# Performance work log

Hardware: AMD Instinct MI355X
Metric: run time of the kernel (lower is better)

Reference implementation:

```python
import jax, jax.numpy as jnp
import numpy as np

N, IN_DIM, E, H, L, M = 65536, 512, 128, 4, 2, 256
DH = E // H  # 32

def _gaussian_orthogonal(m, d, rng):
    # FAVOR+ gaussian orthogonal random matrix (performer_pytorch, scaling=0)
    blocks = []
    for _ in range((m + d - 1) // d):
        q, _ = np.linalg.qr(rng.normal(size=(d, d)))
        blocks.append(q.T)
    mat = np.concatenate(blocks)[:m]
    mult = np.linalg.norm(rng.normal(size=(m, d)), axis=1)
    return (mult[:, None] * mat).astype(np.float32)

def setup_inputs() -> dict:
    rng = np.random.default_rng(0)
    r = lambda *s: jnp.asarray(rng.normal(size=s, scale=0.02), jnp.float32)
    z = lambda *s: jnp.zeros(s, jnp.float32)
    o = lambda *s: jnp.ones(s, jnp.float32)
    return dict(
        x=jnp.asarray(rng.normal(size=(N, IN_DIM)), dtype=jnp.float32),
        Wpin=r(IN_DIM, E), bpin=z(E),
        lag=o(L, E), lab=z(L, E),                    # performer inner pre-LN (attn)
        Wq=r(L, E, E), Wk=r(L, E, E), Wv=r(L, E, E), # qkv (no bias in performer_pytorch)
        Wo=r(L, E, E), bo=z(L, E),                   # attn to_out
        lbg=o(L, E), lbb=z(L, E),                    # performer inner pre-LN (ff)
        Wf1=r(L, E, 4 * E), bf1=z(L, 4 * E),         # performer inner GELU FFN
        Wf2=r(L, 4 * E, E), bf2=z(L, E),
        Wpo=r(L, E, E), bpo=z(L, E),                 # PerformerSelfAttention.out_proj
        n1g=o(L, E), n1b=z(L, E),                    # block norm1
        Wn1=r(L, E, 4 * E), bn1=z(L, 4 * E),         # block ReLU FFN
        Wn2=r(L, 4 * E, E), bn2=z(L, E),
        n2g=o(L, E), n2b=z(L, E),                    # block norm2
        Wc=r(E, 1), bc=z(1),                         # classifier
        proj=jnp.stack([jnp.asarray(_gaussian_orthogonal(M, DH, rng)) for _ in range(L)]),
    )

def _ln(x, g, b, eps=1e-5):
    mu = x.mean(-1, keepdims=True)
    var = ((x - mu) ** 2).mean(-1, keepdims=True)
    return (x - mu) * jax.lax.rsqrt(var + eps) * g + b

def _softmax_kernel(data, proj, is_query, eps=1e-4):
    # data: [1,H,N,DH]; proj: [M,DH]  (performer_pytorch softmax_kernel)
    dn = data.shape[-1] ** -0.25
    ratio = proj.shape[0] ** -0.5
    dd = jnp.einsum('bhnd,md->bhnm', data * dn, proj)
    diag = (data ** 2).sum(-1, keepdims=True) * 0.5 * (dn * dn)
    stab = jnp.max(dd, -1, keepdims=True) if is_query else jnp.max(dd)
    return ratio * (jnp.exp(dd - diag - stab) + eps)

def _linear_attn(qf, kf, v):
    # non-causal FAVOR+: O(N*M*DH)
    D = jnp.einsum('bhnm,bhm->bhn', qf, kf.sum(-2))          # denominator
    ctx = jnp.einsum('bhnm,bhnd->bhmd', kf, v)               # [1,H,M,DH]
    return jnp.einsum('bhnm,bhmd->bhnd', qf, ctx) / D[..., None]

def _forward(x, Wpin, bpin, lag, lab, Wq, Wk, Wv, Wo, bo, lbg, lbb,
             Wf1, bf1, Wf2, bf2, Wpo, bpo, n1g, n1b, Wn1, bn1, Wn2, bn2,
             n2g, n2b, Wc, bc, proj):
    h = (x @ Wpin + bpin)[None]  # [1,N,E]
    split = lambda t: t.reshape(1, -1, H, DH).transpose(0, 2, 1, 3)
    for l in range(L):
        # --- inner Performer (depth=1): pre-LN attn + pre-LN GELU FFN, residuals ---
        y = _ln(h, lag[l], lab[l])
        q, k, v = split(y @ Wq[l]), split(y @ Wk[l]), split(y @ Wv[l])
        qf = _softmax_kernel(q, proj[l], True)
        kf = _softmax_kernel(k, proj[l], False)
        a = _linear_attn(qf, kf, v).transpose(0, 2, 1, 3).reshape(1, -1, E)
        h1 = h + (a @ Wo[l] + bo[l])
        y2 = _ln(h1, lbg[l], lbb[l])
        h2 = h1 + (jax.nn.gelu(y2 @ Wf1[l] + bf1[l], approximate=False) @ Wf2[l] + bf2[l])
        # --- outer block: post-LN residual attn + post-LN ReLU FFN ---
        attn_out = h2 @ Wpo[l] + bpo[l]
        h = _ln(h + attn_out, n1g[l], n1b[l])
        ffn = jax.nn.relu(h @ Wn1[l] + bn1[l]) @ Wn2[l] + bn2[l]
        h = _ln(h + ffn, n2g[l], n2b[l])
    return jax.nn.sigmoid(h[0] @ Wc + bc)[:, 0]  # [N]

def reference(x, Wpin, bpin, lag, lab, Wq, Wk, Wv, Wo, bo, lbg, lbb,
              Wf1, bf1, Wf2, bf2, Wpo, bpo, n1g, n1b, Wn1, bn1, Wn2, bn2,
              n2g, n2b, Wc, bc, proj):
    return _forward(x, Wpin, bpin, lag, lab, Wq, Wk, Wv, Wo, bo, lbg, lbb,
                    Wf1, bf1, Wf2, bf2, Wpo, bpo, n1g, n1b, Wn1, bn1, Wn2, bn2,
                    n2g, n2b, Wc, bc, proj)
```

## Files before the change

kernel.cpp:

```cpp
#include <hip/hip_runtime.h>
#include <math.h>

#define NTOK  65536
#define EDIM  128
#define HN    4
#define DHD   32
#define MF    256
#define LLAYERS 2
#define INDIM 512
#define FDIM  512
#define CR    512
#define NCHK  (NTOK/CR)

#define DN    0.4204482076268573f
#define DN2   0.17677669529663687f
#define KEPS  1e-4f

typedef unsigned short u16;
typedef unsigned int   u32;
typedef __attribute__((ext_vector_type(8))) __bf16 bf16x8;
typedef __attribute__((ext_vector_type(4))) float  f32x4;

__device__ __forceinline__ u16 f2bf(float f){
  u32 u = __float_as_uint(f);
  u32 r = (u + 0x7fffu + ((u >> 16) & 1u)) >> 16;
  return (u16)r;
}
__device__ __forceinline__ float bf2f(u16 h){ return __uint_as_float(((u32)h) << 16); }

__device__ __forceinline__ void gload_lds16(const void* g, void* l){
  __builtin_amdgcn_global_load_lds(
      (const __attribute__((address_space(1))) u32*)g,
      (__attribute__((address_space(3))) u32*)l, 16, 0, 0);
}

__device__ __forceinline__ unsigned f2ord(float f){
  unsigned u = __float_as_uint(f);
  return (u & 0x80000000u) ? ~u : (u | 0x80000000u);
}
__device__ __forceinline__ float ord2f(unsigned e){
  unsigned u = (e & 0x80000000u) ? (e & 0x7fffffffu) : ~e;
  return __uint_as_float(u);
}

struct PrepArgs {
  const float* Wpin; const float* Wq; const float* Wk; const float* Wv;
  const float* Wo;   const float* Wpo; const float* Wf1; const float* Wf2;
  const float* Wn1;  const float* Wn2; const float* proj;
};

__global__ __launch_bounds__(256) void prep_kernel(PrepArgs a, u16* __restrict__ wts,
                                                   u16* __restrict__ pjb,
                                                   unsigned* __restrict__ stabp)
{
  int idx = blockIdx.x * 256 + threadIdx.x;
  if (idx == 0) { stabp[0] = 0x007FFFFFu; stabp[1] = 0x007FFFFFu; }
  const float* sp; u16* dp; int r, K, J;
  if      (idx <  65536) { sp = a.Wpin; dp = wts;          r = idx;          K = 512; J = 128; }
  else if (idx <  98304) { sp = a.Wq;   dp = wts +  65536; r = idx -  65536; K = 128; J = 128; }
  else if (idx < 131072) { sp = a.Wk;   dp = wts +  98304; r = idx -  98304; K = 128; J = 128; }
  else if (idx < 163840) { sp = a.Wv;   dp = wts + 131072; r = idx - 131072; K = 128; J = 128; }
  else if (idx < 196608) { sp = a.Wo;   dp = wts + 163840; r = idx - 163840; K = 128; J = 128; }
  else if (idx < 229376) { sp = a.Wpo;  dp = wts + 196608; r = idx - 196608; K = 128; J = 128; }
  else if (idx < 360448) { sp = a.Wf1;  dp = wts + 229376; r = idx - 229376; K = 128; J = 512; }
  else if (idx < 491520) { sp = a.Wf2;  dp = wts + 360448; r = idx - 360448; K = 512; J = 128; }
  else if (idx < 622592) { sp = a.Wn1;  dp = wts + 491520; r = idx - 491520; K = 128; J = 512; }
  else if (idx < 753664) { sp = a.Wn2;  dp = wts + 622592; r = idx - 622592; K = 512; J = 128; }
  else { int p = idx - 753664; pjb[p] = f2bf(a.proj[p] * DN); return; }
  int kj = K * J;
  int l = r / kj, rr = r - l * kj;
  int j = rr / K, k = rr - j * K;
  dp[r] = f2bf(sp[(size_t)l * kj + (size_t)k * J + j]);
}

template<int LNM, bool A32, bool MULTI>
__global__ __launch_bounds__(256, 4) void gemm_f(
    const u16* __restrict__ A, const float* __restrict__ Af,
    const u16* __restrict__ Bt,
    const float* __restrict__ bias, const u16* __restrict__ res,
    u16* __restrict__ outRaw, int K, int J, int op,
    const float* __restrict__ g1, const float* __restrict__ b1, u16* __restrict__ outL1,
    u16* __restrict__ outAux,
    const float* __restrict__ Wcp, const float* __restrict__ bcp, float* __restrict__ outCls)
{
  __shared__ __align__(16) u16 pool[18432];
  __shared__ float lnred[2][2][32][2];
  u16* Al = pool;
  u16* Bl = pool + 6144;
  const int tid  = threadIdx.x;
  const int lane = tid & 63;
  const int w    = tid >> 6;
  const int wr   = w >> 1, wc = w & 1;
  const int n0   = blockIdx.x * 64;
  const int jb   = MULTI ? 0 : blockIdx.y * 128;
  const u16* Bu  = MULTI ? (Bt + (size_t)blockIdx.y * 32768) : Bt;

  f32x4 acc[2][4];
#pragma unroll
  for (int m = 0; m < 2; ++m)
#pragma unroll
    for (int n = 0; n < 4; ++n) acc[m][n] = (f32x4){0.f, 0.f, 0.f, 0.f};

  const int srow = lane >> 2;
  const int skg  = (lane & 3) ^ ((lane >> 3) & 3);

  auto stageB = [&](int buf, int k0) {
#pragma unroll
    for (int i = 0; i < 2; ++i) {
      const int rb = 2 * w + i;
      gload_lds16(Bu + (size_t)(jb + rb * 16 + srow) * K + k0 + skg * 8,
                  &Bl[buf * 4096 + rb * 512]);
    }
  };
  auto stageA16 = [&](int buf, int k0) {
    gload_lds16(A + (size_t)(n0 + w * 16 + srow) * K + k0 + skg * 8,
                &Al[buf * 2048 + w * 512]);
  };

  const int r16f = lane & 15;
  const int kgl  = (lane >> 4) ^ ((lane >> 1) & 3);
  const int foff = r16f * 32 + kgl * 8;

  auto compute = [&](int cur) {
    bf16x8 af[2], bfg[4];
#pragma unroll
    for (int m = 0; m < 2; ++m)
      af[m]  = *reinterpret_cast<const bf16x8*>(&Al[cur * 2048 + (wr * 2 + m) * 512 + foff]);
#pragma unroll
    for (int n = 0; n < 4; ++n)
      bfg[n] = *reinterpret_cast<const bf16x8*>(&Bl[cur * 4096 + (wc * 4 + n) * 512 + foff]);
#pragma unroll
    for (int m = 0; m < 2; ++m)
#pragma unroll
      for (int n = 0; n < 4; ++n)
        acc[m][n] = __builtin_amdgcn_mfma_f32_16x16x32_bf16(af[m], bfg[n], acc[m][n], 0, 0, 0);
  };

  if constexpr (A32) {
    constexpr int T = 16;
    float4 fA[3][2];
    const int r = tid >> 2, hf = tid & 3;
    auto loadA = [&](int slot, int k0) {
      const float* gp = Af + (size_t)(n0 + r) * 512 + k0 + hf * 8;
      fA[slot][0] = ((const float4*)gp)[0];
      fA[slot][1] = ((const float4*)gp)[1];
    };
    const int rbA = r >> 4, r16A = r & 15, swzA = (r16A >> 1) & 3;
    auto writeA = [&](int slot, int buf) {
      uint4 p0;
      p0.x = (u32)f2bf(fA[slot][0].x) | ((u32)f2bf(fA[slot][0].y) << 16);
      p0.y = (u32)f2bf(fA[slot][0].z) | ((u32)f2bf(fA[slot][0].w) << 16);
      p0.z = (u32)f2bf(fA[slot][1].x) | ((u32)f2bf(fA[slot][1].y) << 16);
      p0.w = (u32)f2bf(fA[slot][1].z) | ((u32)f2bf(fA[slot][1].w) << 16);
      *reinterpret_cast<uint4*>(&Al[buf * 2048 + rbA * 512 + r16A * 32 + (hf ^ swzA) * 8]) = p0;
    };
    loadA(0, 0); loadA(1, 32); loadA(2, 64);
    stageB(0, 0); stageB(1, 32);
    asm volatile("s_waitcnt vmcnt(8)" ::: "memory");
    writeA(0, 0);
#pragma unroll
    for (int t = 0; t < T; ++t) {
      if (t + 2 < T) asm volatile("s_waitcnt vmcnt(4) lgkmcnt(0)" ::: "memory");
      else           asm volatile("s_waitcnt vmcnt(0) lgkmcnt(0)" ::: "memory");
      __builtin_amdgcn_s_barrier();
      if (t + 1 < T) writeA((t + 1) % 3, (t + 1) % 3);
      if (t + 3 < T) loadA((t + 3) % 3, (t + 3) * 32);
      if (t + 2 < T) stageB((t + 2) % 3, (t + 2) * 32);
      compute(t % 3);
    }
    __builtin_amdgcn_s_barrier();
  } else {
    const int T = K >> 5;
    stageA16(0, 0); stageB(0, 0);
    stageA16(1, 32); stageB(1, 32);
    for (int t = 0; t < T; ++t) {
      if (t + 1 < T) asm volatile("s_waitcnt vmcnt(3) lgkmcnt(0)" ::: "memory");
      else           asm volatile("s_waitcnt vmcnt(0) lgkmcnt(0)" ::: "memory");
      __builtin_amdgcn_s_barrier();
      int cur = t % 3;
      if (t + 2 < T) { stageA16((t + 2) % 3, (t + 2) * 32); stageB((t + 2) % 3, (t + 2) * 32); }
      compute(cur);
    }
    __builtin_amdgcn_s_barrier();
  }

  const int colb = jb + wc * 64 + (lane & 15);
  const int rowb = n0 + wr * 32 + (lane >> 4) * 4;
  float bv[4];
#pragma unroll
  for (int n = 0; n < 4; ++n) bv[n] = bias ? bias[colb + n * 16] : 0.f;

  float v[2][4][4];
#pragma unroll
  for (int m = 0; m < 2; ++m)
#pragma unroll
    for (int n = 0; n < 4; ++n)
#pragma unroll
      for (int j = 0; j < 4; ++j) {
        float t = acc[m][n][j] + bv[n];
        if (op == 1)      t = 0.5f * t * (1.f + erff(t * 0.70710678118654752f));
        else if (op == 2) t = fmaxf(t, 0.f);
        if (res) t += bf2f(res[(size_t)(rowb + m * 16 + j) * J + colb + n * 16]);
        v[m][n][j] = t;
      }

  if constexpr (MULTI) {
    if (blockIdx.y == 2) {
      u16* tb = pool;
#pragma unroll
      for (int m = 0; m < 2; ++m)
#pragma unroll
        for (int n = 0; n < 4; ++n)
#pragma unroll
          for (int j = 0; j < 4; ++j)
            tb[(wc * 64 + n * 16 + (lane & 15)) * 72 + wr * 32 + m * 16 + (lane >> 4) * 4 + j]
                = f2bf(v[m][n][j]);
      __syncthreads();
      { const int c2 = tid >> 1, hf2 = tid & 1;
        const uint4* src = reinterpret_cast<const uint4*>(&tb[c2 * 72 + hf2 * 32]);
        uint4* dst = reinterpret_cast<uint4*>(outAux + (size_t)c2 * NTOK + n0 + hf2 * 32);
        dst[0] = src[0]; dst[1] = src[1]; dst[2] = src[2]; dst[3] = src[3]; }
      return;
    }
    u16* out0 = (blockIdx.y == 0) ? outRaw : outL1;
#pragma unroll
    for (int m = 0; m < 2; ++m)
#pragma unroll
      for (int n = 0; n < 4; ++n)
#pragma unroll
        for (int j = 0; j < 4; ++j)
          out0[(size_t)(rowb + m * 16 + j) * J + colb + n * 16] = f2bf(v[m][n][j]);
    return;
  }

  if (outRaw) {
#pragma unroll
    for (int m = 0; m < 2; ++m)
#pragma unroll
      for (int n = 0; n < 4; ++n)
#pragma unroll
        for (int j = 0; j < 4; ++j)
          outRaw[(size_t)(rowb + m * 16 + j) * J + colb + n * 16] = f2bf(v[m][n][j]);
  }

  if constexpr (LNM > 0 && !MULTI) {
    auto ln_apply = [&](const float* gp, const float* bp) {
      float rs[2][4], rq[2][4];
#pragma unroll
      for (int m = 0; m < 2; ++m)
#pragma unroll
        for (int j = 0; j < 4; ++j) {
          float s = 0.f, q = 0.f;
#pragma unroll
          for (int n = 0; n < 4; ++n) { float t = v[m][n][j]; s += t; q += t * t; }
          rs[m][j] = s; rq[m][j] = q;
        }
#pragma unroll
      for (int o = 1; o < 16; o <<= 1)
#pragma unroll
        for (int m = 0; m < 2; ++m)
#pragma unroll
          for (int j = 0; j < 4; ++j) {
            rs[m][j] += __shfl_xor(rs[m][j], o);
            rq[m][j] += __shfl_xor(rq[m][j], o);
          }
      __syncthreads();
      if ((lane & 15) == 0) {
#pragma unroll
        for (int m = 0; m < 2; ++m)
#pragma unroll
          for (int j = 0; j < 4; ++j) {
            int rloc = m * 16 + (lane >> 4) * 4 + j;
            lnred[wr][wc][rloc][0] = rs[m][j];
            lnred[wr][wc][rloc][1] = rq[m][j];
          }
      }
      __syncthreads();
      float gg[4], bb[4];
#pragma unroll
      for (int n = 0; n < 4; ++n) { gg[n] = gp[colb + n * 16]; bb[n] = bp[colb + n * 16]; }
#pragma unroll
      for (int m = 0; m < 2; ++m)
#pragma unroll
        for (int j = 0; j < 4; ++j) {
          int rloc = m * 16 + (lane >> 4) * 4 + j;
          float ts = rs[m][j] + lnred[wr][wc ^ 1][rloc][0];
          float tq = rq[m][j] + lnred[wr][wc ^ 1][rloc][1];
          float mu = ts * (1.f / 128.f);
          float rsig = rsqrtf(tq * (1.f / 128.f) - mu * mu + 1e-5f);
#pragma unroll
          for (int n = 0; n < 4; ++n)
            v[m][n][j] = (v[m][n][j] - mu) * rsig * gg[n] + bb[n];
        }
    };

    ln_apply(g1, b1);
    if (outL1) {
#pragma unroll
      for (int m = 0; m < 2; ++m)
#pragma unroll
        for (int n = 0; n < 4; ++n)
#pragma unroll
          for (int j = 0; j < 4; ++j)
            outL1[(size_t)(rowb + m * 16 + j) * J + colb + n * 16] = f2bf(v[m][n][j]);
    }
  }
}

template<int LNM, int ACT>
__global__ __launch_bounds__(256, 2) void ffn_f(
    const u16* __restrict__ A, const u16* __restrict__ W1t, const float* __restrict__ fb1p,
    const u16* __restrict__ W2t, const float* __restrict__ fb2p,
    const u16* __restrict__ res, u16* __restrict__ out,
    const float* __restrict__ g1, const float* __restrict__ bt1,
    u16* __restrict__ outL2, const float* __restrict__ g2, const float* __restrict__ bt2,
    const float* __restrict__ Wcp, const float* __restrict__ bcp, float* __restrict__ outCls)
{
  __shared__ __align__(16) u16 As[4][2048];
  __shared__ __align__(16) u16 Hs[4][2048];
  __shared__ __align__(16) u16 Bs[3][4096];
  __shared__ float lnred[2][2][32][2];
  const int tid  = threadIdx.x;
  const int lane = tid & 63;
  const int w    = tid >> 6;
  const int wr   = w >> 1, wc = w & 1;
  const int n0   = blockIdx.x * 64;

  const int srow = lane >> 2;
  const int skg  = (lane & 3) ^ ((lane >> 3) & 3);
  const int r16f = lane & 15;
  const int kgl  = (lane >> 4) ^ ((lane >> 1) & 3);
  const int foff = r16f * 32 + kgl * 8;

#pragma unroll
  for (int rb = 0; rb < 4; ++rb)
    gload_lds16(A + (size_t)(n0 + rb * 16 + srow) * EDIM + w * 32 + skg * 8, &As[w][rb * 512]);

  auto stageB = [&](int buf, int st) {
    const int c = st >> 3, p = (st >> 2) & 1, kt = st & 3;
    const u16* base; size_t rstride; int kb0;
    if (p == 0) { base = W1t + (size_t)c * 128 * 128; rstride = 128; kb0 = kt * 32; }
    else        { base = W2t;                          rstride = 512; kb0 = c * 128 + kt * 32; }
#pragma unroll
    for (int i = 0; i < 2; ++i) {
      const int rb = 2 * w + i;
      gload_lds16(base + (size_t)(rb * 16 + srow) * rstride + kb0 + skg * 8, &Bs[buf][rb * 512]);
    }
  };

  stageB(0, 0);
  stageB(1, 1);

  f32x4 acc1[2][4], acc2[2][4];
#pragma unroll
  for (int m = 0; m < 2; ++m)
#pragma unroll
    for (int n = 0; n < 4; ++n) acc2[m][n] = (f32x4){0.f, 0.f, 0.f, 0.f};

#pragma unroll
  for (int st = 0; st < 32; ++st) {
    const int c = st >> 3, p = (st >> 2) & 1, kt = st & 3;
    if (st + 1 < 32) asm volatile("s_waitcnt vmcnt(2) lgkmcnt(0)" ::: "memory");
    else             asm volatile("s_waitcnt vmcnt(0) lgkmcnt(0)" ::: "memory");
    __builtin_amdgcn_s_barrier();
    if (st + 2 < 32) stageB((st + 2) % 3, st + 2);
    if ((st & 7) == 0) {
#pragma unroll
      for (int m = 0; m < 2; ++m)
#pragma unroll
        for (int n = 0; n < 4; ++n) acc1[m][n] = (f32x4){0.f, 0.f, 0.f, 0.f};
    }
    const u16* Asrc = p ? &Hs[kt][0] : &As[kt][0];
    const u16* Bc = &Bs[st % 3][0];
    bf16x8 af[2], bfg[4];
#pragma unroll
    for (int m = 0; m < 2; ++m) af[m]  = *reinterpret_cast<const bf16x8*>(&Asrc[(wr * 2 + m) * 512 + foff]);
#pragma unroll
    for (int n = 0; n < 4; ++n) bfg[n] = *reinterpret_cast<const bf16x8*>(&Bc[(wc * 4 + n) * 512 + foff]);
    if (p == 0) {
#pragma unroll
      for (int m = 0; m < 2; ++m)
#pragma unroll
        for (int n = 0; n < 4; ++n)
          acc1[m][n] = __builtin_amdgcn_mfma_f32_16x16x32_bf16(af[m], bfg[n], acc1[m][n], 0, 0, 0);
    } else {
#pragma unroll
      for (int m = 0; m < 2; ++m)
#pragma unroll
        for (int n = 0; n < 4; ++n)
          acc2[m][n] = __builtin_amdgcn_mfma_f32_16x16x32_bf16(af[m], bfg[n], acc2[m][n], 0, 0, 0);
    }
    if ((st & 7) == 3) {
      float fb[4];
#pragma unroll
      for (int n = 0; n < 4; ++n) fb[n] = fb1p[c * 128 + wc * 64 + n * 16 + (lane & 15)];
#pragma unroll
      for (int m = 0; m < 2; ++m)
#pragma unroll
        for (int n = 0; n < 4; ++n)
#pragma unroll
          for (int j = 0; j < 4; ++j) {
            float t = acc1[m][n][j] + fb[n];
            if (ACT == 1) t = 0.5f * t * (1.f + erff(t * 0.70710678118654752f));
            else          t = fmaxf(t, 0.f);
            const int r16 = (lane >> 4) * 4 + j;
            const int rb  = wr * 2 + m;
            const int q   = wc * 64 + n * 16 + (lane & 15);
            const int ts  = q >> 5, ql = q & 31;
            const int s   = (ql >> 3) ^ ((r16 >> 1) & 3);
            Hs[ts][rb * 512 + r16 * 32 + s * 8 + (ql & 7)] = f2bf(t);
          }
    }
  }

  const int colb = wc * 64 + (lane & 15);
  const int rowb = n0 + wr * 32 + (lane >> 4) * 4;
  float fb[4];
#pragma unroll
  for (int n = 0; n < 4; ++n) fb[n] = fb2p[colb + n * 16];
  float v[2][4][4];
#pragma unroll
  for (int m = 0; m < 2; ++m)
#pragma unroll
    for (int n = 0; n < 4; ++n)
#pragma unroll
      for (int j = 0; j < 4; ++j) {
        float t = acc2[m][n][j] + fb[n];
        t += bf2f(res[(size_t)(rowb + m * 16 + j) * EDIM + colb + n * 16]);
        v[m][n][j] = t;
      }

  auto ln_apply = [&](const float* gp, const float* bp) {
    float rs[2][4], rq[2][4];
#pragma unroll
    for (int m = 0; m < 2; ++m)
#pragma unroll
      for (int j = 0; j < 4; ++j) {
        float s = 0.f, q = 0.f;
#pragma unroll
        for (int n = 0; n < 4; ++n) { float t = v[m][n][j]; s += t; q += t * t; }
        rs[m][j] = s; rq[m][j] = q;
      }
#pragma unroll
    for (int o = 1; o < 16; o <<= 1)
#pragma unroll
      for (int m = 0; m < 2; ++m)
#pragma unroll
        for (int j = 0; j < 4; ++j) {
          rs[m][j] += __shfl_xor(rs[m][j], o);
          rq[m][j] += __shfl_xor(rq[m][j], o);
        }
    __syncthreads();
    if ((lane & 15) == 0) {
#pragma unroll
      for (int m = 0; m < 2; ++m)
#pragma unroll
        for (int j = 0; j < 4; ++j) {
          int rloc = m * 16 + (lane >> 4) * 4 + j;
          lnred[wr][wc][rloc][0] = rs[m][j];
          lnred[wr][wc][rloc][1] = rq[m][j];
        }
    }
    __syncthreads();
    float gg[4], bb[4];
#pragma unroll
    for (int n = 0; n < 4; ++n) { gg[n] = gp[colb + n * 16]; bb[n] = bp[colb + n * 16]; }
#pragma unroll
    for (int m = 0; m < 2; ++m)
#pragma unroll
      for (int j = 0; j < 4; ++j) {
        int rloc = m * 16 + (lane >> 4) * 4 + j;
        float ts = rs[m][j] + lnred[wr][wc ^ 1][rloc][0];
        float tq = rq[m][j] + lnred[wr][wc ^ 1][rloc][1];
        float mu = ts * (1.f / 128.f);
        float rsig = rsqrtf(tq * (1.f / 128.f) - mu * mu + 1e-5f);
#pragma unroll
        for (int n = 0; n < 4; ++n)
          v[m][n][j] = (v[m][n][j] - mu) * rsig * gg[n] + bb[n];
      }
  };

  if constexpr (LNM > 0) ln_apply(g1, bt1);
#pragma unroll
  for (int m = 0; m < 2; ++m)
#pragma unroll
    for (int n = 0; n < 4; ++n)
#pragma unroll
      for (int j = 0; j < 4; ++j)
        out[(size_t)(rowb + m * 16 + j) * EDIM + colb + n * 16] = f2bf(v[m][n][j]);

  if constexpr (LNM == 2) {
    ln_apply(g2, bt2);
#pragma unroll
    for (int m = 0; m < 2; ++m)
#pragma unroll
      for (int n = 0; n < 4; ++n)
#pragma unroll
        for (int j = 0; j < 4; ++j)
          outL2[(size_t)(rowb + m * 16 + j) * EDIM + colb + n * 16] = f2bf(v[m][n][j]);
  }
  if constexpr (LNM == 3) {
    const float bc0 = bcp[0];
    float wv[4];
#pragma unroll
    for (int n = 0; n < 4; ++n) wv[n] = Wcp[colb + n * 16];
    float dp[2][4];
#pragma unroll
    for (int m = 0; m < 2; ++m)
#pragma unroll
      for (int j = 0; j < 4; ++j) {
        float s = 0.f;
#pragma unroll
        for (int n = 0; n < 4; ++n) s += v[m][n][j] * wv[n];
        dp[m][j] = s;
      }
#pragma unroll
    for (int o = 1; o < 16; o <<= 1)
#pragma unroll
      for (int m = 0; m < 2; ++m)
#pragma unroll
        for (int j = 0; j < 4; ++j) dp[m][j] += __shfl_xor(dp[m][j], o);
    __syncthreads();
    if ((lane & 15) == 0) {
#pragma unroll
      for (int m = 0; m < 2; ++m)
#pragma unroll
        for (int j = 0; j < 4; ++j)
          lnred[wr][wc][m * 16 + (lane >> 4) * 4 + j][0] = dp[m][j];
    }
    __syncthreads();
    if (wc == 0 && (lane & 15) == 0) {
#pragma unroll
      for (int m = 0; m < 2; ++m)
#pragma unroll
        for (int j = 0; j < 4; ++j) {
          int rloc = m * 16 + (lane >> 4) * 4 + j;
          float t = dp[m][j] + lnred[wr][1][rloc][0] + bc0;
          outCls[n0 + wr * 32 + rloc] = 1.f / (1.f + expf(-t));
        }
    }
  }
}

__global__ __launch_bounds__(256) void smax_kernel(
    const u16* __restrict__ Km, const u16* __restrict__ pjb,
    unsigned* __restrict__ stabp)
{
  __shared__ float wred[4];
  const int tid = threadIdx.x, lane = tid & 63, w = tid >> 6;
  const int h = blockIdx.y;
  const int n0 = blockIdx.x * 256 + w * 64;
  const int g = lane >> 4, c = lane & 15;
  bf16x8 af[4];
#pragma unroll
  for (int mf = 0; mf < 4; ++mf)
    af[mf] = *reinterpret_cast<const bf16x8*>(
        Km + (size_t)(n0 + mf * 16 + c) * EDIM + h * DHD + g * 8);
  float lm = -3.4e38f;
  const f32x4 z = (f32x4){0.f, 0.f, 0.f, 0.f};
#pragma unroll
  for (int jf = 0; jf < 16; ++jf) {
    bf16x8 bfg = *reinterpret_cast<const bf16x8*>(pjb + (jf * 16 + c) * DHD + g * 8);
#pragma unroll
    for (int mf = 0; mf < 4; ++mf) {
      f32x4 d = __builtin_amdgcn_mfma_f32_16x16x32_bf16(af[mf], bfg, z, 0, 0, 0);
      lm = fmaxf(lm, fmaxf(fmaxf(d[0], d[1]), fmaxf(d[2], d[3])));
    }
  }
#pragma unroll
  for (int o = 1; o < 64; o <<= 1) lm = fmaxf(lm, __shfl_xor(lm, o));
  if (lane == 0) wred[w] = lm;
  __syncthreads();
  if (tid == 0)
    atomicMax(stabp, f2ord(fmaxf(fmaxf(wred[0], wred[1]), fmaxf(wred[2], wred[3]))));
}

__global__ __launch_bounds__(256) void ctxk_kernel(
    const u16* __restrict__ Km, const u16* __restrict__ VT,
    const u16* __restrict__ pjb, const unsigned* __restrict__ stabp,
    float* __restrict__ pctx, float* __restrict__ pks)
{
  __shared__ __align__(16) u16 kfT[256 * 40];
  const int tid = threadIdx.x, lane = tid & 63, w = tid >> 6;
  const int h = blockIdx.y, ch = blockIdx.x;
  const int n0 = ch * CR;
  const int g = lane >> 4, c = lane & 15;
  const float stab = ord2f(*stabp);
  const f32x4 z = (f32x4){0.f, 0.f, 0.f, 0.f};

  bf16x8 pf[4];
#pragma unroll
  for (int jf = 0; jf < 4; ++jf)
    pf[jf] = *reinterpret_cast<const bf16x8*>(pjb + ((w * 4 + jf) * 16 + c) * DHD + g * 8);

  f32x4 cacc[4][2];
#pragma unroll
  for (int mf = 0; mf < 4; ++mf)
#pragma unroll
    for (int df = 0; df < 2; ++df) cacc[mf][df] = z;
  float ksacc[4] = {0.f, 0.f, 0.f, 0.f};

  for (int s = 0; s < CR / 32; ++s) {
    const int rbase = n0 + s * 32;
    bf16x8 af[2];
    float s2[2];
#pragma unroll
    for (int rf = 0; rf < 2; ++rf) {
      af[rf] = *reinterpret_cast<const bf16x8*>(
          Km + (size_t)(rbase + rf * 16 + c) * EDIM + h * DHD + g * 8);
      uint4 ui = *reinterpret_cast<const uint4*>(&af[rf]);
      u32 wd[4] = {ui.x, ui.y, ui.z, ui.w};
      float ss = 0.f;
#pragma unroll
      for (int i = 0; i < 4; ++i) {
        float a = bf2f((u16)(wd[i] & 0xffff)), b = bf2f((u16)(wd[i] >> 16));
        ss += a * a + b * b;
      }
      ss += __shfl_xor(ss, 16); ss += __shfl_xor(ss, 32);
      s2[rf] = ss;
    }
#pragma unroll
    for (int rf = 0; rf < 2; ++rf) {
      float dg[4];
#pragma unroll
      for (int r = 0; r < 4; ++r)
        dg[r] = 0.5f * DN2 * __shfl(s2[rf], (lane & 48) | (4 * g + r)) + stab;
#pragma unroll
      for (int jf = 0; jf < 4; ++jf) {
        f32x4 d = __builtin_amdgcn_mfma_f32_16x16x32_bf16(af[rf], pf[jf], z, 0, 0, 0);
        u16 b0 = f2bf(__expf(d[0] - dg[0]) + KEPS);
        u16 b1 = f2bf(__expf(d[1] - dg[1]) + KEPS);
        u16 b2 = f2bf(__expf(d[2] - dg[2]) + KEPS);
        u16 b3 = f2bf(__expf(d[3] - dg[3]) + KEPS);
        uint2 pk;
        pk.x = (u32)b0 | ((u32)b1 << 16);
        pk.y = (u32)b2 | ((u32)b3 << 16);
        *reinterpret_cast<uint2*>(&kfT[(size_t)(w * 64 + jf * 16 + c) * 40 + rf * 16 + 4 * g]) = pk;
        ksacc[jf] += bf2f(b0) + bf2f(b1) + bf2f(b2) + bf2f(b3);
      }
    }
#pragma unroll
    for (int mf = 0; mf < 4; ++mf) {
      bf16x8 a = *reinterpret_cast<const bf16x8*>(&kfT[(size_t)(w * 64 + mf * 16 + c) * 40 + g * 8]);
#pragma unroll
      for (int df = 0; df < 2; ++df) {
        bf16x8 b = *reinterpret_cast<const bf16x8*>(
            VT + (size_t)(h * DHD + df * 16 + c) * NTOK + rbase + g * 8);
        cacc[mf][df] = __builtin_amdgcn_mfma_f32_16x16x32_bf16(a, b, cacc[mf][df], 0, 0, 0);
      }
    }
  }
#pragma unroll
  for (int jf = 0; jf < 4; ++jf) {
    float vv = ksacc[jf];
    vv += __shfl_xor(vv, 16); vv += __shfl_xor(vv, 32);
    if (g == 0) pks[((size_t)h * NCHK + ch) * MF + w * 64 + jf * 16 + c] = vv;
  }
#pragma unroll
  for (int mf = 0; mf < 4; ++mf)
#pragma unroll
    for (int df = 0; df < 2; ++df)
#pragma unroll
      for (int r = 0; r < 4; ++r) {
        int m = w * 64 + mf * 16 + 4 * g + r;
        int d = df * 16 + c;
        pctx[(((size_t)h * NCHK + ch) * MF + m) * DHD + d] = cacc[mf][df][r];
      }
}

__global__ __launch_bounds__(256) void reduce_all(
    const float* __restrict__ pctx, const float* __restrict__ pks,
    u16* __restrict__ ctxT, float* __restrict__ ksg)
{
  int idx = blockIdx.x * 256 + threadIdx.x;
  if (idx < HN * MF * DHD) {
    int h = idx >> 13, md = idx & 8191;
    int m = md >> 5, d = md & 31;
    float s = 0.f;
    for (int c = 0; c < NCHK; ++c) s += pctx[((size_t)h * NCHK + c) * 8192 + md];
    ctxT[(size_t)h * 8192 + d * MF + m] = f2bf(s);
  } else {
    int i2 = idx - HN * MF * DHD;
    if (i2 < HN * MF) {
      int h = i2 >> 8, m = i2 & 255;
      float s = 0.f;
      for (int c = 0; c < NCHK; ++c) s += pks[((size_t)h * NCHK + c) * MF + m];
      ksg[i2] = s;
    }
  }
}

__global__ __launch_bounds__(256) void qout_kernel(
    const u16* __restrict__ Qm, const u16* __restrict__ pjb,
    const u16* __restrict__ ctxT, const float* __restrict__ ksg,
    u16* __restrict__ Am)
{
  __shared__ __align__(16) u16 qfs[4][32 * 40];
  const int tid = threadIdx.x, lane = tid & 63, w = tid >> 6;
  const int h = blockIdx.y;
  const int n0 = blockIdx.x * 128 + w * 32;
  const int g = lane >> 4, c = lane & 15;
  const f32x4 z = (f32x4){0.f, 0.f, 0.f, 0.f};

  bf16x8 af[2];
  float s2[2];
#pragma unroll
  for (int rf = 0; rf < 2; ++rf) {
    af[rf] = *reinterpret_cast<const bf16x8*>(
        Qm + (size_t)(n0 + rf * 16 + c) * EDIM + h * DHD + g * 8);
    uint4 ui = *reinterpret_cast<const uint4*>(&af[rf]);
    u32 wd[4] = {ui.x, ui.y, ui.z, ui.w};
    float ss = 0.f;
#pragma unroll
    for (int i = 0; i < 4; ++i) {
      float a = bf2f((u16)(wd[i] & 0xffff)), b = bf2f((u16)(wd[i] >> 16));
      ss += a * a + b * b;
    }
    ss += __shfl_xor(ss, 16); ss += __shfl_xor(ss, 32);
    s2[rf] = ss;
  }

  float rmax[2][4];
#pragma unroll
  for (int rf = 0; rf < 2; ++rf)
#pragma unroll
    for (int r = 0; r < 4; ++r) rmax[rf][r] = -3.4e38f;
#pragma unroll
  for (int jf = 0; jf < 16; ++jf) {
    bf16x8 b = *reinterpret_cast<const bf16x8*>(pjb + (jf * 16 + c) * DHD + g * 8);
#pragma unroll
    for (int rf = 0; rf < 2; ++rf) {
      f32x4 d = __builtin_amdgcn_mfma_f32_16x16x32_bf16(af[rf], b, z, 0, 0, 0);
#pragma unroll
      for (int r = 0; r < 4; ++r) rmax[rf][r] = fmaxf(rmax[rf][r], d[r]);
    }
  }
#pragma unroll
  for (int rf = 0; rf < 2; ++rf)
#pragma unroll
    for (int r = 0; r < 4; ++r) {
      float vv = rmax[rf][r];
      vv = fmaxf(vv, __shfl_xor(vv, 1)); vv = fmaxf(vv, __shfl_xor(vv, 2));
      vv = fmaxf(vv, __shfl_xor(vv, 4)); vv = fmaxf(vv, __shfl_xor(vv, 8));
      rmax[rf][r] = vv;
    }
  float crow[2][4];
#pragma unroll
  for (int rf = 0; rf < 2; ++rf)
#pragma unroll
    for (int r = 0; r < 4; ++r)
      crow[rf][r] = 0.5f * DN2 * __shfl(s2[rf], (lane & 48) | (4 * g + r)) + rmax[rf][r];

  f32x4 oacc[2][2];
#pragma unroll
  for (int rf = 0; rf < 2; ++rf)
#pragma unroll
    for (int df = 0; df < 2; ++df) oacc[rf][df] = z;
  float Dacc[2][4];
#pragma unroll
  for (int rf = 0; rf < 2; ++rf)
#pragma unroll
    for (int r = 0; r < 4; ++r) Dacc[rf][r] = 0.f;

  for (int ks = 0; ks < 8; ++ks) {
#pragma unroll
    for (int jj = 0; jj < 2; ++jj) {
      const int jf = ks * 2 + jj;
      bf16x8 b = *reinterpret_cast<const bf16x8*>(pjb + (jf * 16 + c) * DHD + g * 8);
      const float ksv = ksg[h * MF + jf * 16 + c];
#pragma unroll
      for (int rf = 0; rf < 2; ++rf) {
        f32x4 d = __builtin_amdgcn_mfma_f32_16x16x32_bf16(af[rf], b, z, 0, 0, 0);
#pragma unroll
        for (int r = 0; r < 4; ++r) {
          float q = __expf(d[r] - crow[rf][r]) + KEPS;
          u16 qb_ = f2bf(q);
          qfs[w][(rf * 16 + 4 * g + r) * 40 + jj * 16 + c] = qb_;
          Dacc[rf][r] += bf2f(qb_) * ksv;
        }
      }
    }
#pragma unroll
    for (int rf = 0; rf < 2; ++rf) {
      bf16x8 a = *reinterpret_cast<const bf16x8*>(&qfs[w][(rf * 16 + c) * 40 + g * 8]);
#pragma unroll
      for (int df = 0; df < 2; ++df) {
        bf16x8 bc = *reinterpret_cast<const bf16x8*>(
            ctxT + (size_t)(h * DHD + df * 16 + c) * MF + ks * 32 + g * 8);
        oacc[rf][df] = __builtin_amdgcn_mfma_f32_16x16x32_bf16(a, bc, oacc[rf][df], 0, 0, 0);
      }
    }
  }
#pragma unroll
  for (int rf = 0; rf < 2; ++rf)
#pragma unroll
    for (int r = 0; r < 4; ++r) {
      float vv = Dacc[rf][r];
      vv += __shfl_xor(vv, 1); vv += __shfl_xor(vv, 2);
      vv += __shfl_xor(vv, 4); vv += __shfl_xor(vv, 8);
      Dacc[rf][r] = vv;
    }
#pragma unroll
  for (int rf = 0; rf < 2; ++rf)
#pragma unroll
    for (int df = 0; df < 2; ++df)
#pragma unroll
      for (int r = 0; r < 4; ++r)
        Am[(size_t)(n0 + rf * 16 + 4 * g + r) * EDIM + h * DHD + df * 16 + c] =
            f2bf(oacc[rf][df][r] / Dacc[rf][r]);
}

extern "C" void kernel_launch(void* const* d_in, const int* in_sizes, int n_in,
                              void* d_out, int out_size, void* d_ws, size_t ws_size,
                              hipStream_t stream)
{
  const float* x    = (const float*)d_in[0];
  const float* Wpin = (const float*)d_in[1];
  const float* bpin = (const float*)d_in[2];
  const float* lag  = (const float*)d_in[3];
  const float* lab  = (const float*)d_in[4];
  const float* Wq   = (const float*)d_in[5];
  const float* Wk   = (const float*)d_in[6];
  const float* Wv   = (const float*)d_in[7];
  const float* Wo   = (const float*)d_in[8];
  const float* bo   = (const float*)d_in[9];
  const float* lbg  = (const float*)d_in[10];
  const float* lbb  = (const float*)d_in[11];
  const float* Wf1  = (const float*)d_in[12];
  const float* bf1  = (const float*)d_in[13];
  const float* Wf2  = (const float*)d_in[14];
  const float* bf2  = (const float*)d_in[15];
  const float* Wpo  = (const float*)d_in[16];
  const float* bpo  = (const float*)d_in[17];
  const float* n1g  = (const float*)d_in[18];
  const float* n1b  = (const float*)d_in[19];
  const float* Wn1  = (const float*)d_in[20];
  const float* bn1  = (const float*)d_in[21];
  const float* Wn2  = (const float*)d_in[22];
  const float* bn2  = (const float*)d_in[23];
  const float* n2g  = (const float*)d_in[24];
  const float* n2b  = (const float*)d_in[25];
  const float* Wc   = (const float*)d_in[26];
  const float* bc   = (const float*)d_in[27];
  const float* proj = (const float*)d_in[28];

  size_t off = 0;
  char* base = (char*)d_ws;
  auto alloc = [&](size_t bytes) -> void* {
    void* p = base + off;
    off += (bytes + 255) & ~(size_t)255;
    return p;
  };
  u16* hb  = (u16*)alloc((size_t)NTOK * EDIM * 2);
  u16* yb  = (u16*)alloc((size_t)NTOK * EDIM * 2);
  u16* qb  = (u16*)alloc((size_t)NTOK * EDIM * 2);
  u16* kb  = (u16*)alloc((size_t)NTOK * EDIM * 2);
  u16* vb  = (u16*)alloc((size_t)NTOK * EDIM * 2);
  u16* VT  = (u16*)alloc((size_t)HN * DHD * NTOK * 2);
  u16* pjb = (u16*)alloc((size_t)LLAYERS * MF * DHD * 2);
  u16* ctxT = (u16*)alloc((size_t)HN * DHD * MF * 2);
  float* ksg  = (float*)alloc((size_t)HN * MF * 4);
  float* pctx = (float*)alloc((size_t)HN * NCHK * MF * DHD * 4);
  float* pks  = (float*)alloc((size_t)HN * NCHK * MF * 4);
  unsigned* stabp = (unsigned*)alloc(256);
  u16* wts = (u16*)alloc((size_t)753664 * 2);

  u16* Wpint = wts;
  auto Wqt  = [&](int l){ return wts +  65536 + (size_t)l * 16384; };
  auto Wot  = [&](int l){ return wts + 163840 + (size_t)l * 16384; };
  auto Wpot = [&](int l){ return wts + 196608 + (size_t)l * 16384; };
  auto Wf1t = [&](int l){ return wts + 229376 + (size_t)l * 65536; };
  auto Wf2t = [&](int l){ return wts + 360448 + (size_t)l * 65536; };
  auto Wn1t = [&](int l){ return wts + 491520 + (size_t)l * 65536; };
  auto Wn2t = [&](int l){ return wts + 622592 + (size_t)l * 65536; };

  PrepArgs pa{Wpin, Wq, Wk, Wv, Wo, Wpo, Wf1, Wf2, Wn1, Wn2, proj};
  prep_kernel<<<3008, 256, 0, stream>>>(pa, wts, pjb, stabp);

  gemm_f<1, true, false><<<dim3(NTOK / 64, 1), 256, 0, stream>>>(
      nullptr, x, Wpint, bpin, nullptr, hb, INDIM, EDIM, 0,
      lag, lab, yb, nullptr, nullptr, nullptr, nullptr);

  for (int l = 0; l < LLAYERS; ++l) {
    const u16* pjl = pjb + (size_t)l * MF * DHD;

    gemm_f<0, false, true><<<dim3(NTOK / 64, 3), 256, 0, stream>>>(
        yb, nullptr, Wqt(l), nullptr, nullptr, qb, EDIM, EDIM, 0,
        nullptr, nullptr, kb, VT, nullptr, nullptr, nullptr);

    smax_kernel<<<dim3(NTOK / 256, HN), 256, 0, stream>>>(kb, pjl, stabp + l);
    ctxk_kernel<<<dim3(NCHK, HN), 256, 0, stream>>>(kb, VT, pjl, stabp + l, pctx, pks);
    reduce_all<<<132, 256, 0, stream>>>(pctx, pks, ctxT, ksg);
    qout_kernel<<<dim3(NTOK / 128, HN), 256, 0, stream>>>(qb, pjl, ctxT, ksg, yb);

    gemm_f<1, false, false><<<dim3(NTOK / 64, 1), 256, 0, stream>>>(
        yb, nullptr, Wot(l), bo + l * EDIM, hb, qb, EDIM, EDIM, 0,
        lbg + l * EDIM, lbb + l * EDIM, kb, nullptr, nullptr, nullptr, nullptr);
    ffn_f<0, 1><<<NTOK / 64, 256, 0, stream>>>(
        kb, Wf1t(l), bf1 + l * FDIM, Wf2t(l), bf2 + l * EDIM, qb, vb,
        nullptr, nullptr, nullptr, nullptr, nullptr, nullptr, nullptr, nullptr);
    gemm_f<1, false, false><<<dim3(NTOK / 64, 1), 256, 0, stream>>>(
        vb, nullptr, Wpot(l), bpo + l * EDIM, hb, nullptr, EDIM, EDIM, 0,
        n1g + l * EDIM, n1b + l * EDIM, hb, nullptr, nullptr, nullptr, nullptr);
    if (l < LLAYERS - 1) {
      ffn_f<2, 2><<<NTOK / 64, 256, 0, stream>>>(
          hb, Wn1t(l), bn1 + l * FDIM, Wn2t(l), bn2 + l * EDIM, hb, hb,
          n2g + l * EDIM, n2b + l * EDIM,
          yb, lag + (l + 1) * EDIM, lab + (l + 1) * EDIM,
          nullptr, nullptr, nullptr);
    } else {
      ffn_f<3, 2><<<NTOK / 64, 256, 0, stream>>>(
          hb, Wn1t(l), bn1 + l * FDIM, Wn2t(l), bn2 + l * EDIM, hb, hb,
          n2g + l * EDIM, n2b + l * EDIM,
          nullptr, nullptr, nullptr,
          Wc, bc, (float*)d_out);
    }
  }
}
```

Measured before the change: 563.5 us.

## Fuse projection GEMM plus LayerNorm into following FFN kernel; swizzle block order

Merges each 128x128 projection GEMM (attn to_out and out_proj), with its bias, residual and LayerNorm, into the front of the following FFN kernel. The normalized tile is written straight into LDS as the FFN's A operand, which removes two kernel launches per layer and the HBM round trip of the intermediate activations. Block indices are also swizzled in groups of 8 across the grid in both GEMM kernels. The fused kernel now holds an extra accumulator set and v0 registers, which may add register pressure at 2 waves/SIMD, and the gemm_f activation op path is removed.

After: 514.8 us. -8.6%, faster.

```diff
diff --git a/kernel.cpp b/kernel.cpp
--- a/kernel.cpp
+++ b/kernel.cpp
@@ -91,7 +91,10 @@
   const int lane = tid & 63;
   const int w    = tid >> 6;
   const int wr   = w >> 1, wc = w & 1;
-  const int n0   = blockIdx.x * 64;
+  const int bid  = blockIdx.x;
+  const int nwg8 = gridDim.x >> 3;
+  const int bsw  = (bid & 7) * nwg8 + (bid >> 3);
+  const int n0   = bsw * 64;
   const int jb   = MULTI ? 0 : blockIdx.y * 128;
   const u16* Bu  = MULTI ? (Bt + (size_t)blockIdx.y * 32768) : Bt;
 
@@ -198,8 +201,6 @@
 #pragma unroll
       for (int j = 0; j < 4; ++j) {
         float t = acc[m][n][j] + bv[n];
-        if (op == 1)      t = 0.5f * t * (1.f + erff(t * 0.70710678118654752f));
-        else if (op == 2) t = fmaxf(t, 0.f);
         if (res) t += bf2f(res[(size_t)(rowb + m * 16 + j) * J + colb + n * 16]);
         v[m][n][j] = t;
       }
@@ -244,57 +245,53 @@
   }
 
   if constexpr (LNM > 0 && !MULTI) {
-    auto ln_apply = [&](const float* gp, const float* bp) {
-      float rs[2][4], rq[2][4];
+    float rs[2][4], rq[2][4];
+#pragma unroll
+    for (int m = 0; m < 2; ++m)
+#pragma unroll
+      for (int j = 0; j < 4; ++j) {
+        float s = 0.f, q = 0.f;
+#pragma unroll
+        for (int n = 0; n < 4; ++n) { float t = v[m][n][j]; s += t; q += t * t; }
+        rs[m][j] = s; rq[m][j] = q;
+      }
+#pragma unroll
+    for (int o = 1; o < 16; o <<= 1)
 #pragma unroll
       for (int m = 0; m < 2; ++m)
 #pragma unroll
         for (int j = 0; j < 4; ++j) {
-          float s = 0.f, q = 0.f;
-#pragma unroll
-          for (int n = 0; n < 4; ++n) { float t = v[m][n][j]; s += t; q += t * t; }
-          rs[m][j] = s; rq[m][j] = q;
+          rs[m][j] += __shfl_xor(rs[m][j], o);
+          rq[m][j] += __shfl_xor(rq[m][j], o);
         }
-#pragma unroll
-      for (int o = 1; o < 16; o <<= 1)
-#pragma unroll
-        for (int m = 0; m < 2; ++m)
-#pragma unroll
-          for (int j = 0; j < 4; ++j) {
-            rs[m][j] += __shfl_xor(rs[m][j], o);
-            rq[m][j] += __shfl_xor(rq[m][j], o);
-          }
-      __syncthreads();
-      if ((lane & 15) == 0) {
-#pragma unroll
-        for (int m = 0; m < 2; ++m)
-#pragma unroll
-          for (int j = 0; j < 4; ++j) {
-            int rloc = m * 16 + (lane >> 4) * 4 + j;
-            lnred[wr][wc][rloc][0] = rs[m][j];
-            lnred[wr][wc][rloc][1] = rq[m][j];
-          }
-      }
-      __syncthreads();
-      float gg[4], bb[4];
-#pragma unroll
-      for (int n = 0; n < 4; ++n) { gg[n] = gp[colb + n * 16]; bb[n] = bp[colb + n * 16]; }
+    __syncthreads();
+    if ((lane & 15) == 0) {
 #pragma unroll
       for (int m = 0; m < 2; ++m)
 #pragma unroll
         for (int j = 0; j < 4; ++j) {
           int rloc = m * 16 + (lane >> 4) * 4 + j;
-          float ts = rs[m][j] + lnred[wr][wc ^ 1][rloc][0];
-          float tq = rq[m][j] + lnred[wr][wc ^ 1][rloc][1];
-          float mu = ts * (1.f / 128.f);
-          float rsig = rsqrtf(tq * (1.f / 128.f) - mu * mu + 1e-5f);
-#pragma unroll
-          for (int n = 0; n < 4; ++n)
-            v[m][n][j] = (v[m][n][j] - mu) * rsig * gg[n] + bb[n];
+          lnred[wr][wc][rloc][0] = rs[m][j];
+          lnred[wr][wc][rloc][1] = rq[m][j];
         }
-    };
-
-    ln_apply(g1, b1);
+    }
+    __syncthreads();
+    float gg[4], bb[4];
+#pragma unroll
+    for (int n = 0; n < 4; ++n) { gg[n] = g1[colb + n * 16]; bb[n] = b1[colb + n * 16]; }
+#pragma unroll
+    for (int m = 0; m < 2; ++m)
+#pragma unroll
+      for (int j = 0; j < 4; ++j) {
+        int rloc = m * 16 + (lane >> 4) * 4 + j;
+        float ts = rs[m][j] + lnred[wr][wc ^ 1][rloc][0];
+        float tq = rq[m][j] + lnred[wr][wc ^ 1][rloc][1];
+        float mu = ts * (1.f / 128.f);
+        float rsig = rsqrtf(tq * (1.f / 128.f) - mu * mu + 1e-5f);
+#pragma unroll
+        for (int n = 0; n < 4; ++n)
+          v[m][n][j] = (v[m][n][j] - mu) * rsig * gg[n] + bb[n];
+      }
     if (outL1) {
 #pragma unroll
       for (int m = 0; m < 2; ++m)
@@ -307,11 +304,14 @@
   }
 }
 
-template<int LNM, int ACT>
-__global__ __launch_bounds__(256, 2) void ffn_f(
-    const u16* __restrict__ A, const u16* __restrict__ W1t, const float* __restrict__ fb1p,
+template<bool RESPOST, int ACT, int LNM>
+__global__ __launch_bounds__(256, 2) void mega_f(
+    const u16* __restrict__ A0, const u16* __restrict__ W0t,
+    const float* __restrict__ b0p, const u16* __restrict__ res0,
+    const float* __restrict__ g0, const float* __restrict__ bg0,
+    const u16* __restrict__ W1t, const float* __restrict__ fb1p,
     const u16* __restrict__ W2t, const float* __restrict__ fb2p,
-    const u16* __restrict__ res, u16* __restrict__ out,
+    u16* __restrict__ out,
     const float* __restrict__ g1, const float* __restrict__ bt1,
     u16* __restrict__ outL2, const float* __restrict__ g2, const float* __restrict__ bt2,
     const float* __restrict__ Wcp, const float* __restrict__ bcp, float* __restrict__ outCls)
@@ -324,23 +324,31 @@
   const int lane = tid & 63;
   const int w    = tid >> 6;
   const int wr   = w >> 1, wc = w & 1;
-  const int n0   = blockIdx.x * 64;
+  const int bid  = blockIdx.x;
+  const int bsw  = (bid & 7) * (gridDim.x >> 3) + (bid >> 3);
+  const int n0   = bsw * 64;
 
   const int srow = lane >> 2;
   const int skg  = (lane & 3) ^ ((lane >> 3) & 3);
   const int r16f = lane & 15;
   const int kgl  = (lane >> 4) ^ ((lane >> 1) & 3);
   const int foff = r16f * 32 + kgl * 8;
+  const int colb = wc * 64 + (lane & 15);
+  const int rowb = n0 + wr * 32 + (lane >> 4) * 4;
 
 #pragma unroll
   for (int rb = 0; rb < 4; ++rb)
-    gload_lds16(A + (size_t)(n0 + rb * 16 + srow) * EDIM + w * 32 + skg * 8, &As[w][rb * 512]);
+    gload_lds16(A0 + (size_t)(n0 + rb * 16 + srow) * EDIM + w * 32 + skg * 8, &As[w][rb * 512]);
 
   auto stageB = [&](int buf, int st) {
-    const int c = st >> 3, p = (st >> 2) & 1, kt = st & 3;
     const u16* base; size_t rstride; int kb0;
-    if (p == 0) { base = W1t + (size_t)c * 128 * 128; rstride = 128; kb0 = kt * 32; }
-    else        { base = W2t;                          rstride = 512; kb0 = c * 128 + kt * 32; }
+    if (st < 4) { base = W0t; rstride = 128; kb0 = st * 32; }
+    else {
+      int s2 = st - 4;
+      int c = s2 >> 3, p = (s2 >> 2) & 1, kt = s2 & 3;
+      if (p == 0) { base = W1t + (size_t)c * 16384; rstride = 128; kb0 = kt * 32; }
+      else        { base = W2t;                      rstride = 512; kb0 = c * 128 + kt * 32; }
+    }
 #pragma unroll
     for (int i = 0; i < 2; ++i) {
       const int rb = 2 * w + i;
@@ -351,70 +359,154 @@
   stageB(0, 0);
   stageB(1, 1);
 
-  f32x4 acc1[2][4], acc2[2][4];
+  f32x4 acc0[2][4], acc1[2][4], acc2[2][4];
 #pragma unroll
   for (int m = 0; m < 2; ++m)
 #pragma unroll
-    for (int n = 0; n < 4; ++n) acc2[m][n] = (f32x4){0.f, 0.f, 0.f, 0.f};
-
-#pragma unroll
-  for (int st = 0; st < 32; ++st) {
-    const int c = st >> 3, p = (st >> 2) & 1, kt = st & 3;
-    if (st + 1 < 32) asm volatile("s_waitcnt vmcnt(2) lgkmcnt(0)" ::: "memory");
+    for (int n = 0; n < 4; ++n) { acc0[m][n] = (f32x4){0.f,0.f,0.f,0.f}; acc2[m][n] = (f32x4){0.f,0.f,0.f,0.f}; }
+
+  float v0[2][4][4];
+
+#pragma unroll
+  for (int st = 0; st < 36; ++st) {
+    if (st + 1 < 36) asm volatile("s_waitcnt vmcnt(2) lgkmcnt(0)" ::: "memory");
     else             asm volatile("s_waitcnt vmcnt(0) lgkmcnt(0)" ::: "memory");
     __builtin_amdgcn_s_barrier();
-    if (st + 2 < 32) stageB((st + 2) % 3, st + 2);
-    if ((st & 7) == 0) {
+    if (st + 2 < 36) stageB((st + 2) % 3, st + 2);
+
+    if (st < 4) {
+      const u16* Bc = &Bs[st % 3][0];
+      bf16x8 af[2], bfg[4];
+#pragma unroll
+      for (int m = 0; m < 2; ++m) af[m]  = *reinterpret_cast<const bf16x8*>(&As[st][(wr * 2 + m) * 512 + foff]);
+#pragma unroll
+      for (int n = 0; n < 4; ++n) bfg[n] = *reinterpret_cast<const bf16x8*>(&Bc[(wc * 4 + n) * 512 + foff]);
 #pragma unroll
       for (int m = 0; m < 2; ++m)
 #pragma unroll
-        for (int n = 0; n < 4; ++n) acc1[m][n] = (f32x4){0.f, 0.f, 0.f, 0.f};
-    }
-    const u16* Asrc = p ? &Hs[kt][0] : &As[kt][0];
-    const u16* Bc = &Bs[st % 3][0];
-    bf16x8 af[2], bfg[4];
-#pragma unroll
-    for (int m = 0; m < 2; ++m) af[m]  = *reinterpret_cast<const bf16x8*>(&Asrc[(wr * 2 + m) * 512 + foff]);
-#pragma unroll
-    for (int n = 0; n < 4; ++n) bfg[n] = *reinterpret_cast<const bf16x8*>(&Bc[(wc * 4 + n) * 512 + foff]);
-    if (p == 0) {
-#pragma unroll
-      for (int m = 0; m < 2; ++m)
-#pragma unroll
         for (int n = 0; n < 4; ++n)
-          acc1[m][n] = __builtin_amdgcn_mfma_f32_16x16x32_bf16(af[m], bfg[n], acc1[m][n], 0, 0, 0);
-    } else {
-#pragma unroll
-      for (int m = 0; m < 2; ++m)
-#pragma unroll
-        for (int n = 0; n < 4; ++n)
-          acc2[m][n] = __builtin_amdgcn_mfma_f32_16x16x32_bf16(af[m], bfg[n], acc2[m][n], 0, 0, 0);
-    }
-    if ((st & 7) == 3) {
-      float fb[4];
-#pragma unroll
-      for (int n = 0; n < 4; ++n) fb[n] = fb1p[c * 128 + wc * 64 + n * 16 + (lane & 15)];
-#pragma unroll
-      for (int m = 0; m < 2; ++m)
-#pragma unroll
-        for (int n = 0; n < 4; ++n)
+          acc0[m][n] = __builtin_amdgcn_mfma_f32_16x16x32_bf16(af[m], bfg[n], acc0[m][n], 0, 0, 0);
+      if (st == 3) {
+        float bv0[4];
+#pragma unroll
+        for (int n = 0; n < 4; ++n) bv0[n] = b0p[colb + n * 16];
+#pragma unroll
+        for (int m = 0; m < 2; ++m)
+#pragma unroll
+          for (int n = 0; n < 4; ++n)
+#pragma unroll
+            for (int j = 0; j < 4; ++j)
+              v0[m][n][j] = acc0[m][n][j] + bv0[n]
+                  + bf2f(res0[(size_t)(rowb + m * 16 + j) * EDIM + colb + n * 16]);
+        float rs[2][4], rq[2][4];
+#pragma unroll
+        for (int m = 0; m < 2; ++m)
 #pragma unroll
           for (int j = 0; j < 4; ++j) {
-            float t = acc1[m][n][j] + fb[n];
-            if (ACT == 1) t = 0.5f * t * (1.f + erff(t * 0.70710678118654752f));
-            else          t = fmaxf(t, 0.f);
+            float s = 0.f, q = 0.f;
+#pragma unroll
+            for (int n = 0; n < 4; ++n) { float t = v0[m][n][j]; s += t; q += t * t; }
+            rs[m][j] = s; rq[m][j] = q;
+          }
+#pragma unroll
+        for (int o = 1; o < 16; o <<= 1)
+#pragma unroll
+          for (int m = 0; m < 2; ++m)
+#pragma unroll
+            for (int j = 0; j < 4; ++j) {
+              rs[m][j] += __shfl_xor(rs[m][j], o);
+              rq[m][j] += __shfl_xor(rq[m][j], o);
+            }
+        __syncthreads();
+        if ((lane & 15) == 0) {
+#pragma unroll
+          for (int m = 0; m < 2; ++m)
+#pragma unroll
+            for (int j = 0; j < 4; ++j) {
+              int rloc = m * 16 + (lane >> 4) * 4 + j;
+              lnred[wr][wc][rloc][0] = rs[m][j];
+              lnred[wr][wc][rloc][1] = rq[m][j];
+            }
+        }
+        __syncthreads();
+        float gg[4], bb[4];
+#pragma unroll
+        for (int n = 0; n < 4; ++n) { gg[n] = g0[colb + n * 16]; bb[n] = bg0[colb + n * 16]; }
+#pragma unroll
+        for (int m = 0; m < 2; ++m)
+#pragma unroll
+          for (int j = 0; j < 4; ++j) {
+            int rloc = m * 16 + (lane >> 4) * 4 + j;
+            float ts = rs[m][j] + lnred[wr][wc ^ 1][rloc][0];
+            float tq = rq[m][j] + lnred[wr][wc ^ 1][rloc][1];
+            float mu = ts * (1.f / 128.f);
+            float rsig = rsqrtf(tq * (1.f / 128.f) - mu * mu + 1e-5f);
             const int r16 = (lane >> 4) * 4 + j;
             const int rb  = wr * 2 + m;
-            const int q   = wc * 64 + n * 16 + (lane & 15);
-            const int ts  = q >> 5, ql = q & 31;
-            const int s   = (ql >> 3) ^ ((r16 >> 1) & 3);
-            Hs[ts][rb * 512 + r16 * 32 + s * 8 + (ql & 7)] = f2bf(t);
+#pragma unroll
+            for (int n = 0; n < 4; ++n) {
+              float lnv = (v0[m][n][j] - mu) * rsig * gg[n] + bb[n];
+              const int q = wc * 64 + n * 16 + (lane & 15);
+              const int ts2 = q >> 5, ql = q & 31;
+              const int s = (ql >> 3) ^ ((r16 >> 1) & 3);
+              As[ts2][rb * 512 + r16 * 32 + s * 8 + (ql & 7)] = f2bf(lnv);
+              if (RESPOST) v0[m][n][j] = lnv;
+            }
           }
-    }
-  }
-
-  const int colb = wc * 64 + (lane & 15);
-  const int rowb = n0 + wr * 32 + (lane >> 4) * 4;
+      }
+    } else {
+      const int s2 = st - 4;
+      const int c = s2 >> 3, p = (s2 >> 2) & 1, kt = s2 & 3;
+      if ((s2 & 7) == 0) {
+#pragma unroll
+        for (int m = 0; m < 2; ++m)
+#pragma unroll
+          for (int n = 0; n < 4; ++n) acc1[m][n] = (f32x4){0.f, 0.f, 0.f, 0.f};
+      }
+      const u16* Asrc = p ? &Hs[kt][0] : &As[kt][0];
+      const u16* Bc = &Bs[st % 3][0];
+      bf16x8 af[2], bfg[4];
+#pragma unroll
+      for (int m = 0; m < 2; ++m) af[m]  = *reinterpret_cast<const bf16x8*>(&Asrc[(wr * 2 + m) * 512 + foff]);
+#pragma unroll
+      for (int n = 0; n < 4; ++n) bfg[n] = *reinterpret_cast<const bf16x8*>(&Bc[(wc * 4 + n) * 512 + foff]);
+      if (p == 0) {
+#pragma unroll
+        for (int m = 0; m < 2; ++m)
+#pragma unroll
+          for (int n = 0; n < 4; ++n)
+            acc1[m][n] = __builtin_amdgcn_mfma_f32_16x16x32_bf16(af[m], bfg[n], acc1[m][n], 0, 0, 0);
+      } else {
+#pragma unroll
+        for (int m = 0; m < 2; ++m)
+#pragma unroll
+          for (int n = 0; n < 4; ++n)
+            acc2[m][n] = __builtin_amdgcn_mfma_f32_16x16x32_bf16(af[m], bfg[n], acc2[m][n], 0, 0, 0);
+      }
+      if ((s2 & 7) == 3) {
+        float fb[4];
+#pragma unroll
+        for (int n = 0; n < 4; ++n) fb[n] = fb1p[c * 128 + wc * 64 + n * 16 + (lane & 15)];
+#pragma unroll
+        for (int m = 0; m < 2; ++m)
+#pragma unroll
+          for (int n = 0; n < 4; ++n)
+#pragma unroll
+            for (int j = 0; j < 4; ++j) {
+              float t = acc1[m][n][j] + fb[n];
+              if (ACT == 1) t = 0.5f * t * (1.f + erff(t * 0.70710678118654752f));
+              else          t = fmaxf(t, 0.f);
+              const int r16 = (lane >> 4) * 4 + j;
+              const int rb  = wr * 2 + m;
+              const int q   = wc * 64 + n * 16 + (lane & 15);
+              const int ts2 = q >> 5, ql = q & 31;
+              const int s   = (ql >> 3) ^ ((r16 >> 1) & 3);
+              Hs[ts2][rb * 512 + r16 * 32 + s * 8 + (ql & 7)] = f2bf(t);
+            }
+      }
+    }
+  }
+
   float fb[4];
 #pragma unroll
   for (int n = 0; n < 4; ++n) fb[n] = fb2p[colb + n * 16];
@@ -424,11 +516,8 @@
 #pragma unroll
     for (int n = 0; n < 4; ++n)
 #pragma unroll
-      for (int j = 0; j < 4; ++j) {
-        float t = acc2[m][n][j] + fb[n];
-        t += bf2f(res[(size_t)(rowb + m * 16 + j) * EDIM + colb + n * 16]);
-        v[m][n][j] = t;
-      }
+      for (int j = 0; j < 4; ++j)
+        v[m][n][j] = acc2[m][n][j] + fb[n] + v0[m][n][j];
 
   auto ln_apply = [&](const float* gp, const float* bp) {
     float rs[2][4], rq[2][4];
@@ -893,24 +982,22 @@
     reduce_all<<<132, 256, 0, stream>>>(pctx, pks, ctxT, ksg);
     qout_kernel<<<dim3(NTOK / 128, HN), 256, 0, stream>>>(qb, pjl, ctxT, ksg, yb);
 
-    gemm_f<1, false, false><<<dim3(NTOK / 64, 1), 256, 0, stream>>>(
-        yb, nullptr, Wot(l), bo + l * EDIM, hb, qb, EDIM, EDIM, 0,
-        lbg + l * EDIM, lbb + l * EDIM, kb, nullptr, nullptr, nullptr, nullptr);
-    ffn_f<0, 1><<<NTOK / 64, 256, 0, stream>>>(
-        kb, Wf1t(l), bf1 + l * FDIM, Wf2t(l), bf2 + l * EDIM, qb, vb,
+    mega_f<false, 1, 0><<<NTOK / 64, 256, 0, stream>>>(
+        yb, Wot(l), bo + l * EDIM, hb, lbg + l * EDIM, lbb + l * EDIM,
+        Wf1t(l), bf1 + l * FDIM, Wf2t(l), bf2 + l * EDIM, vb,
         nullptr, nullptr, nullptr, nullptr, nullptr, nullptr, nullptr, nullptr);
-    gemm_f<1, false, false><<<dim3(NTOK / 64, 1), 256, 0, stream>>>(
-        vb, nullptr, Wpot(l), bpo + l * EDIM, hb, nullptr, EDIM, EDIM, 0,
-        n1g + l * EDIM, n1b + l * EDIM, hb, nullptr, nullptr, nullptr, nullptr);
+
     if (l < LLAYERS - 1) {
-      ffn_f<2, 2><<<NTOK / 64, 256, 0, stream>>>(
-          hb, Wn1t(l), bn1 + l * FDIM, Wn2t(l), bn2 + l * EDIM, hb, hb,
+      mega_f<true, 2, 2><<<NTOK / 64, 256, 0, stream>>>(
+          vb, Wpot(l), bpo + l * EDIM, hb, n1g + l * EDIM, n1b + l * EDIM,
+          Wn1t(l), bn1 + l * FDIM, Wn2t(l), bn2 + l * EDIM, hb,
           n2g + l * EDIM, n2b + l * EDIM,
           yb, lag + (l + 1) * EDIM, lab + (l + 1) * EDIM,
           nullptr, nullptr, nullptr);
     } else {
-      ffn_f<3, 2><<<NTOK / 64, 256, 0, stream>>>(
-          hb, Wn1t(l), bn1 + l * FDIM, Wn2t(l), bn2 + l * EDIM, hb, hb,
+      mega_f<true, 2, 3><<<NTOK / 64, 256, 0, stream>>>(
+          vb, Wpot(l), bpo + l * EDIM, hb, n1g + l * EDIM, n1b + l * EDIM,
+          Wn1t(l), bn1 + l * FDIM, Wn2t(l), bn2 + l * EDIM, hb,
           n2g + l * EDIM, n2b + l * EDIM,
           nullptr, nullptr, nullptr,
           Wc, bc, (float*)d_out);
```
